# Optimization experiments

Measured on AMD Instinct MI355X. Metric: run time of the kernel, lower is better.

The kernel has to match this reference:

```python
import jax, jax.numpy as jnp
import numpy as np

B, N, HW, PS, FHW = 16, 4096, 224, 8, 56

def _gelu(x):
    return jax.nn.gelu(x, approximate=True)  # tanh approximation, matches nn.GELU(approximate='tanh')

def _conv(x, w, b, stride):
    y = jax.lax.conv_general_dilated(x, w, (stride, stride), [(1, 1), (1, 1)],
                                     dimension_numbers=('NCHW', 'OIHW', 'NCHW'))
    return y + b[None, :, None, None]

def _embed(points):
    # for i in 0..11: append sin(2^i * p) then cos(2^i * p) -> [B,N,48]
    factors = 2.0 ** jnp.arange(12, dtype=points.dtype)
    scaled = points[..., None, :] * factors[:, None]          # [B,N,12,2]
    feats = jnp.concatenate([jnp.sin(scaled), jnp.cos(scaled)], axis=-1)  # [B,N,12,4]
    return feats.reshape(points.shape[0], points.shape[1], 48)

def _extract_patches(fmap, points):
    # fmap [B,C,H,W]; points in [0,1]; bilinear grid_sample, zeros padding, align_corners=True
    Bq, C, H, W = fmap.shape
    centers = points * 2.0 - 1.0
    step = 2.0 / (W - 1)
    half = (PS - 1) / 2.0
    offs = jnp.linspace(-half, half, PS, dtype=fmap.dtype) * step
    offx2d, offy2d = jnp.meshgrid(offs, offs, indexing='ij')   # [ps,ps]
    gx = centers[..., 0][..., None, None] + offx2d             # [B,N,ps,ps]
    gy = centers[..., 1][..., None, None] + offy2d
    # align_corners=True pixel coords
    ix = (gx + 1.0) * 0.5 * (W - 1)
    iy = (gy + 1.0) * 0.5 * (H - 1)
    x0f = jnp.floor(ix); y0f = jnp.floor(iy)
    x0 = x0f.astype(jnp.int32); y0 = y0f.astype(jnp.int32)
    x1 = x0 + 1; y1 = y0 + 1
    wx1 = ix - x0f; wx0 = 1.0 - wx1
    wy1 = iy - y0f; wy0 = 1.0 - wy1
    fflat = fmap.reshape(Bq, C, H * W)

    def corner(xi, yi, w):
        valid = ((xi >= 0) & (xi < W) & (yi >= 0) & (yi < H)).astype(fmap.dtype)
        idx = jnp.clip(yi, 0, H - 1) * W + jnp.clip(xi, 0, W - 1)   # [B,N,ps,ps]
        vals = jax.vmap(lambda f, i: f[:, i])(fflat, idx)           # [B,C,N,ps,ps]
        return vals * (w * valid)[:, None]

    out = (corner(x0, y0, wx0 * wy0) + corner(x1, y0, wx1 * wy0)
           + corner(x0, y1, wx0 * wy1) + corner(x1, y1, wx1 * wy1))  # [B,C,N,ps,ps]
    return out.transpose(0, 2, 1, 3, 4)                              # [B,N,C,ps,ps]

def setup_inputs():
    key = jax.random.key(0)
    ks = jax.random.split(key, 26)
    def w(k, shape):
        fan_in = int(np.prod(shape[1:]))
        return jax.random.normal(k, shape, jnp.float32) * (1.0 / np.sqrt(fan_in))
    inp = {
        'points': jax.random.uniform(ks[0], (B, N, 2), jnp.float32),
        'images': jax.random.normal(ks[1], (B, 3, HW, HW), jnp.float32),
        # plane encoder
        'pw1': w(ks[2], (16, 3, 3, 3)),  'pb1': jnp.zeros((16,), jnp.float32),
        'pw2': w(ks[3], (32, 16, 3, 3)), 'pb2': jnp.zeros((32,), jnp.float32),
        'pw3': w(ks[4], (4, 32, 3, 3)),  'pb3': jnp.zeros((4,), jnp.float32),
        # global encoder
        'gw1': w(ks[5], (4, 3, 3, 3)),   'gb1': jnp.zeros((4,), jnp.float32),
        'gw2': w(ks[6], (8, 4, 3, 3)),   'gb2': jnp.zeros((8,), jnp.float32),
        'gw3': w(ks[7], (16, 8, 3, 3)),  'gb3': jnp.zeros((16,), jnp.float32),
        'gw4': w(ks[8], (32, 16, 3, 3)), 'gb4': jnp.zeros((32,), jnp.float32),
        'gw5': w(ks[9], (64, 32, 3, 3)), 'gb5': jnp.zeros((64,), jnp.float32),
        # point encoder (torch Linear: [out,in])
        'lw1': w(ks[10], (256, 48)),  'lb1': jnp.zeros((256,), jnp.float32),
        'lw2': w(ks[11], (256, 256)), 'lb2': jnp.zeros((256,), jnp.float32),
        # head
        'hw1': w(ks[12], (512, 576)), 'hb1': jnp.zeros((512,), jnp.float32),
        'hw2': w(ks[13], (1, 512)),   'hb2': jnp.zeros((1,), jnp.float32),
    }
    return inp

def reference(points, images, pw1, pb1, pw2, pb2, pw3, pb3,
              gw1, gb1, gw2, gb2, gw3, gb3, gw4, gb4, gw5, gb5,
              lw1, lb1, lw2, lb2, hw1, hb1, hw2, hb2):
    # point branch
    pe = _embed(points)                                         # [B,N,48]
    pf = _gelu(pe @ lw1.T + lb1) @ lw2.T + lb2                  # [B,N,256]
    # plane encoder -> 4x56x56 fmap
    f = _gelu(_conv(images, pw1, pb1, 2))
    f = _gelu(_conv(f, pw2, pb2, 2))
    fmap = _gelu(_conv(f, pw3, pb3, 1))                         # [B,4,56,56]
    # global encoder -> [B,64]
    g = images
    for wg, bg in ((gw1, gb1), (gw2, gb2), (gw3, gb3), (gw4, gb4), (gw5, gb5)):
        g = _gelu(_conv(g, wg, bg, 2))
    gc = g.mean(axis=(2, 3))                                    # AvgPool2d(7)+Flatten -> [B,64]
    gc = jnp.broadcast_to(gc[:, None, :], (points.shape[0], points.shape[1], 64))
    # per-point bilinear patch gather
    patches = _extract_patches(fmap, points).reshape(points.shape[0], points.shape[1], -1)  # [B,N,256]
    fused = jnp.concatenate([pf, patches, gc], axis=-1)         # [B,N,576]
    logit = _gelu(fused @ hw1.T + hb1) @ hw2.T + hb2            # [B,N,1]
    return logit
```

## Files before the change

### kernel.cpp

```cpp
#include <hip/hip_runtime.h>
#include <math.h>

#define BB 16
#define NN 4096
#define M_TOT (BB*NN)
#define TBK 32
#define HBK 64

typedef __attribute__((ext_vector_type(8))) short s8v;
typedef __attribute__((ext_vector_type(4))) float f4v;

__device__ __forceinline__ float gelu_t(float x){
    float u = 1.5957691216057308f * x * (1.0f + 0.044715f*x*x);
    return x / (1.0f + __expf(-u));
}

__device__ __forceinline__ unsigned short f2bf(float f){
    unsigned int u = __float_as_uint(f);
    u += 0x7fffu + ((u >> 16) & 1u);
    return (unsigned short)(u >> 16);
}

#define GLL(src, dst) __builtin_amdgcn_global_load_lds( \
    (const __attribute__((address_space(1))) void*)(src), \
    (__attribute__((address_space(3))) void*)(dst), 16, 0, 0)

template<int CIN, int COUT, int STRIDE, int CHUNK>
__device__ __forceinline__ void conv_dev2(
    const float* __restrict__ in, const float* __restrict__ w,
    const float* __restrict__ bias, float* __restrict__ out,
    int Hin, int Win, int Hout, int Wout, int bx, int by, int b, float* tile)
{
    constexpr int IW = 15*STRIDE + 3;
    constexpr int IH = IW;
    constexpr int PITCH = IW + 1;
    int tid = threadIdx.x;
    int tx = tid & 15, ty = tid >> 4;
    int wo = bx*16 + tx;
    int ho = by*16 + ty;
    int win0 = bx*16*STRIDE - 1;
    int hin0 = by*16*STRIDE - 1;
    bool valid = (wo < Wout) && (ho < Hout);

    float acc[COUT];
    #pragma unroll
    for (int co = 0; co < COUT; ++co) acc[co] = bias[co];

    const float* ib = in + (size_t)(b*CIN)*Hin*Win;
    for (int ci0 = 0; ci0 < CIN; ci0 += CHUNK) {
        __syncthreads();
        for (int idx = tid; idx < CHUNK*IH*IW; idx += 256) {
            int c = idx / (IH*IW), rem = idx - c*(IH*IW);
            int r = rem / IW, cc = rem - r*IW;
            int hi = hin0 + r, wi = win0 + cc;
            float v = 0.f;
            if ((unsigned)hi < (unsigned)Hin && (unsigned)wi < (unsigned)Win)
                v = ib[(size_t)(ci0 + c)*Hin*Win + hi*Win + wi];
            tile[c*IH*PITCH + r*PITCH + cc] = v;
        }
        __syncthreads();
        for (int ci = 0; ci < CHUNK; ++ci) {
            float vv[9];
            const float* tb = tile + ci*IH*PITCH;
            #pragma unroll
            for (int kh = 0; kh < 3; ++kh)
                #pragma unroll
                for (int kw = 0; kw < 3; ++kw)
                    vv[kh*3+kw] = tb[(ty*STRIDE + kh)*PITCH + tx*STRIDE + kw];
            const float* wc = w + (ci0 + ci)*9;
            #pragma unroll
            for (int co = 0; co < COUT; ++co) {
                const float* wp = wc + co*CIN*9;
                #pragma unroll
                for (int k = 0; k < 9; ++k)
                    acc[co] = fmaf(vv[k], wp[k], acc[co]);
            }
        }
    }
    if (valid) {
        size_t obase = ((size_t)b*COUT)*Hout*Wout + (size_t)ho*Wout + wo;
        #pragma unroll
        for (int co = 0; co < COUT; ++co)
            out[obase + (size_t)co*Hout*Wout] = gelu_t(acc[co]);
    }
}

__global__ __launch_bounds__(256) void conv_dual_k(
    const float* __restrict__ in,
    const float* __restrict__ wA, const float* __restrict__ bA,
    const float* __restrict__ wB, const float* __restrict__ bB,
    float* __restrict__ outA, float* __restrict__ outB)
{
    __shared__ float tile[3*33*34];
    const int Hin = 224, Win = 224, Hout = 112, Wout = 112;
    int tid = threadIdx.x;
    int tx = tid & 15, ty = tid >> 4;
    int b = blockIdx.z;
    int wo = blockIdx.x*16 + tx;
    int ho = blockIdx.y*16 + ty;
    int win0 = blockIdx.x*32 - 1;
    int hin0 = blockIdx.y*32 - 1;

    const float* ib = in + (size_t)(b*3)*Hin*Win;
    for (int idx = tid; idx < 3*1089; idx += 256) {
        int c = idx / 1089, rem = idx - c*1089;
        int r = rem / 33, cc = rem - r*33;
        int hi = hin0 + r, wi = win0 + cc;
        float v = 0.f;
        if ((unsigned)hi < (unsigned)Hin && (unsigned)wi < (unsigned)Win)
            v = ib[(size_t)c*Hin*Win + hi*Win + wi];
        tile[c*33*34 + r*34 + cc] = v;
    }
    __syncthreads();

    float accA[16], accB[4];
    #pragma unroll
    for (int co = 0; co < 16; ++co) accA[co] = bA[co];
    #pragma unroll
    for (int co = 0; co < 4; ++co) accB[co] = bB[co];

    #pragma unroll
    for (int ci = 0; ci < 3; ++ci) {
        float vv[9];
        const float* tb = tile + ci*33*34;
        #pragma unroll
        for (int kh = 0; kh < 3; ++kh)
            #pragma unroll
            for (int kw = 0; kw < 3; ++kw)
                vv[kh*3+kw] = tb[(ty*2 + kh)*34 + tx*2 + kw];
        #pragma unroll
        for (int co = 0; co < 16; ++co) {
            const float* wp = wA + co*27 + ci*9;
            #pragma unroll
            for (int k = 0; k < 9; ++k) accA[co] = fmaf(vv[k], wp[k], accA[co]);
        }
        #pragma unroll
        for (int co = 0; co < 4; ++co) {
            const float* wp = wB + co*27 + ci*9;
            #pragma unroll
            for (int k = 0; k < 9; ++k) accB[co] = fmaf(vv[k], wp[k], accB[co]);
        }
    }
    size_t px = (size_t)ho*Wout + wo;
    #pragma unroll
    for (int co = 0; co < 16; ++co)
        outA[((size_t)(b*16 + co))*Hout*Wout + px] = gelu_t(accA[co]);
    #pragma unroll
    for (int co = 0; co < 4; ++co)
        outB[((size_t)(b*4 + co))*Hout*Wout + px] = gelu_t(accB[co]);
}

__global__ __launch_bounds__(256) void conv_pg2_k(
    const float* __restrict__ f1, const float* __restrict__ pw2, const float* __restrict__ pb2, float* __restrict__ f2,
    const float* __restrict__ g1, const float* __restrict__ gw2, const float* __restrict__ gb2, float* __restrict__ g2)
{
    __shared__ float tile[8*33*34];
    int z = blockIdx.z;
    if (z < 32) {
        int b = z >> 1, half = z & 1;
        conv_dev2<16,16,2,8>(f1 + (size_t)b*16*12544, pw2 + half*2304, pb2 + half*16,
                             f2 + ((size_t)(b*32 + half*16))*3136,
                             112,112, 56,56, blockIdx.x, blockIdx.y, 0, tile);
    } else {
        conv_dev2<4,8,2,4>(g1, gw2, gb2, g2, 112,112, 56,56, blockIdx.x, blockIdx.y, z-32, tile);
    }
}

__global__ __launch_bounds__(256) void conv_pg3_k(
    const float* __restrict__ f2, const float* __restrict__ pw3, const float* __restrict__ pb3, float4* __restrict__ fmap4,
    const float* __restrict__ g2, const float* __restrict__ gw3, const float* __restrict__ gb3, float* __restrict__ g3)
{
    __shared__ float tile[8*33*34];
    int z = blockIdx.z;
    if (z < 16) {
        int b = z;
        int idx = blockIdx.x*256 + threadIdx.x;
        if (idx >= 3136) return;
        int ho = idx / 56, wo = idx - ho*56;
        const float* ib = f2 + (size_t)b*32*3136;
        float acc[4];
        #pragma unroll
        for (int co = 0; co < 4; ++co) acc[co] = pb3[co];
        for (int ci = 0; ci < 32; ++ci) {
            const float* ic = ib + (size_t)ci*3136;
            #pragma unroll
            for (int kh = 0; kh < 3; ++kh) {
                int hi = ho - 1 + kh;
                if ((unsigned)hi >= 56u) continue;
                #pragma unroll
                for (int kw = 0; kw < 3; ++kw) {
                    int wi = wo - 1 + kw;
                    if ((unsigned)wi >= 56u) continue;
                    float v = ic[hi*56 + wi];
                    int wofs = ci*9 + kh*3 + kw;
                    #pragma unroll
                    for (int co = 0; co < 4; ++co)
                        acc[co] = fmaf(v, pw3[co*288 + wofs], acc[co]);
                }
            }
        }
        float4 o;
        o.x = gelu_t(acc[0]); o.y = gelu_t(acc[1]);
        o.z = gelu_t(acc[2]); o.w = gelu_t(acc[3]);
        fmap4[(size_t)b*3136 + idx] = o;
    } else {
        if (blockIdx.x >= 4) return;
        int bx = blockIdx.x & 1, by = blockIdx.x >> 1;
        conv_dev2<8,16,2,8>(g2, gw3, gb3, g3, 56,56, 28,28, bx, by, z-16, tile);
    }
}

__global__ __launch_bounds__(256) void g4_k(
    const float* __restrict__ g3, const float* __restrict__ w4,
    const float* __restrict__ b4, float* __restrict__ g4o)
{
    int idx = blockIdx.x*256 + threadIdx.x;
    int co = idx & 31;
    int t = idx >> 5;
    int b = t / 196, px = t - b*196;
    int ho = px / 14, wo = px - ho*14;
    const float* src = g3 + (size_t)b*16*784;
    const float* wp = w4 + co*144;
    float acc = b4[co];
    for (int ci = 0; ci < 16; ++ci) {
        #pragma unroll
        for (int kh = 0; kh < 3; ++kh) {
            int hi = ho*2 - 1 + kh;
            if ((unsigned)hi >= 28u) continue;
            #pragma unroll
            for (int kw = 0; kw < 3; ++kw) {
                int wi = wo*2 - 1 + kw;
                if ((unsigned)wi >= 28u) continue;
                acc = fmaf(src[ci*784 + hi*28 + wi], wp[ci*9 + kh*3 + kw], acc);
            }
        }
    }
    g4o[(size_t)b*6272 + px*32 + co] = gelu_t(acc);
}

__global__ __launch_bounds__(256) void g5_k(
    const float* __restrict__ g4o, const float* __restrict__ w5,
    const float* __restrict__ b5, float* __restrict__ gc)
{
    int idx = blockIdx.x*256 + threadIdx.x;
    int co = idx & 63;
    int t = idx >> 6;
    int b = t / 49, px = t - b*49;
    int ho = px / 7, wo = px - ho*7;
    const float* src = g4o + (size_t)b*6272;
    const float* wp = w5 + co*288;
    float acc = b5[co];
    for (int ci = 0; ci < 32; ++ci) {
        #pragma unroll
        for (int kh = 0; kh < 3; ++kh) {
            int hi = ho*2 - 1 + kh;
            if ((unsigned)hi >= 14u) continue;
            #pragma unroll
            for (int kw = 0; kw < 3; ++kw) {
                int wi = wo*2 - 1 + kw;
                if ((unsigned)wi >= 14u) continue;
                acc = fmaf(src[(hi*14 + wi)*32 + ci], wp[ci*9 + kh*3 + kw], acc);
            }
        }
    }
    atomicAdd(&gc[b*64 + co], gelu_t(acc) * (1.0f/49.0f));
}

__global__ void cvtall_k(const float* __restrict__ lw1, const float* __restrict__ lw2,
                         const float* __restrict__ hw1, unsigned short* __restrict__ blw1,
                         unsigned short* __restrict__ blw2, unsigned short* __restrict__ bhw1,
                         float* __restrict__ out, const float* __restrict__ b2,
                         float* __restrict__ gc){
    int i = blockIdx.x*blockDim.x + threadIdx.x;
    if (i < M_TOT) out[i] = b2[0];
    if (i < 1024) gc[i] = 0.f;
    if (i < 256*64) {
        int r = i >> 6, c = i & 63;
        blw1[i] = (c < 48) ? f2bf(lw1[r*48 + c]) : 0;
        return;
    }
    int j = i - 256*64;
    if (j < 256*256) { blw2[j] = f2bf(lw2[j]); return; }
    j -= 256*256;
    if (j < 512*576) bhw1[j] = f2bf(hw1[j]);
}

__global__ __launch_bounds__(512) void mlp12_k(
    const float* __restrict__ points,
    const unsigned short* __restrict__ W1, const float* __restrict__ b1,
    const unsigned short* __restrict__ W2, const float* __restrict__ b2,
    unsigned short* __restrict__ C,
    const float4* __restrict__ fmap4, const float* __restrict__ gc)
{
    __shared__ unsigned short Hd[128*256];
    int tid = threadIdx.x;
    int wv = tid >> 6, lane = tid & 63;
    int q = lane >> 4, lr = lane & 15;
    int mi = wv >> 2, ni = wv & 3;
    size_t m0 = (size_t)blockIdx.x * 128;

    f4v acc1[4][4];
    #pragma unroll
    for (int i = 0; i < 4; ++i)
        #pragma unroll
        for (int j = 0; j < 4; ++j) acc1[i][j] = (f4v){0.f,0.f,0.f,0.f};

    #pragma unroll
    for (int kb = 0; kb < 2; ++kb) {
        int seg = kb*4 + q;
        s8v a[4], b[4];
        #pragma unroll
        for (int t = 0; t < 4; ++t) {
            size_t m = m0 + mi*64 + t*16 + lr;
            float px = points[m*2], py = points[m*2+1];
            union { s8v v; unsigned short u[8]; } pk;
            #pragma unroll
            for (int j = 0; j < 8; ++j) {
                int k = seg*8 + j;
                unsigned short val = 0;
                if (k < 48) {
                    int i2 = k >> 2, rr = k & 3;
                    float f = (float)(1 << i2);
                    float p = (rr & 1) ? py : px;
                    float s = f * p;
                    val = f2bf((rr < 2) ? __sinf(s) : __cosf(s));
                }
                pk.u[j] = val;
            }
            a[t] = pk.v;
        }
        #pragma unroll
        for (int t = 0; t < 4; ++t) {
            int n = ni*64 + t*16 + lr;
            b[t] = *(const s8v*)(W1 + n*64 + seg*8);
        }
        #pragma unroll
        for (int mt = 0; mt < 4; ++mt)
            #pragma unroll
            for (int nt = 0; nt < 4; ++nt)
                acc1[mt][nt] = __builtin_amdgcn_mfma_f32_16x16x32_bf16(a[mt], b[nt], acc1[mt][nt], 0, 0, 0);
    }
    {
        float b1v[4];
        #pragma unroll
        for (int nt = 0; nt < 4; ++nt) b1v[nt] = b1[ni*64 + nt*16 + lr];
        #pragma unroll
        for (int mt = 0; mt < 4; ++mt)
            #pragma unroll
            for (int r4 = 0; r4 < 4; ++r4) {
                int row = mi*64 + mt*16 + q*4 + r4;
                #pragma unroll
                for (int nt = 0; nt < 4; ++nt) {
                    int col = ni*64 + nt*16 + lr;
                    float v = gelu_t(acc1[mt][nt][r4] + b1v[nt]);
                    int p = (col >> 3) ^ (row & 7);
                    Hd[(row*32 + p)*8 + (col & 7)] = f2bf(v);
                }
            }
    }
    __syncthreads();

    f4v acc2[4][4];
    #pragma unroll
    for (int i = 0; i < 4; ++i)
        #pragma unroll
        for (int j = 0; j < 4; ++j) acc2[i][j] = (f4v){0.f,0.f,0.f,0.f};

    #pragma unroll 2
    for (int kt = 0; kt < 8; ++kt) {
        s8v a[4], b[4];
        #pragma unroll
        for (int t = 0; t < 4; ++t) {
            int n = ni*64 + t*16 + lr;
            b[t] = *(const s8v*)(W2 + (size_t)n*256 + kt*32 + q*8);
        }
        #pragma unroll
        for (int t = 0; t < 4; ++t) {
            int row = mi*64 + t*16 + lr;
            int p = (kt*4 + q) ^ (row & 7);
            a[t] = *(const s8v*)(Hd + (row*32 + p)*8);
        }
        #pragma unroll
        for (int mt = 0; mt < 4; ++mt)
            #pragma unroll
            for (int nt = 0; nt < 4; ++nt)
                acc2[mt][nt] = __builtin_amdgcn_mfma_f32_16x16x32_bf16(a[mt], b[nt], acc2[mt][nt], 0, 0, 0);
    }
    {
        float b2v[4];
        #pragma unroll
        for (int nt = 0; nt < 4; ++nt) b2v[nt] = b2[ni*64 + nt*16 + lr];
        #pragma unroll
        for (int mt = 0; mt < 4; ++mt)
            #pragma unroll
            for (int r4 = 0; r4 < 4; ++r4) {
                size_t m = m0 + mi*64 + mt*16 + q*4 + r4;
                #pragma unroll
                for (int nt = 0; nt < 4; ++nt) {
                    int n = ni*64 + nt*16 + lr;
                    C[m*576 + n] = f2bf(acc2[mt][nt][r4] + b2v[nt]);
                }
            }
    }
    #pragma unroll 2
    for (int it = 0; it < 16; ++it) {
        int task = it*512 + tid;
        int ml = task >> 6, ij = task & 63;
        size_t m = m0 + ml;
        int i = ij >> 3, j = ij & 7;
        int b = (int)(m >> 12);
        float px = points[m*2], py = points[m*2+1];
        float cx = px*2.f - 1.f, cy = py*2.f - 1.f;
        const float step = 2.0f/55.0f;
        float gx = cx + ((float)i - 3.5f)*step;
        float gy = cy + ((float)j - 3.5f)*step;
        float ix = (gx + 1.f)*0.5f*55.f;
        float iy = (gy + 1.f)*0.5f*55.f;
        float x0f = floorf(ix), y0f = floorf(iy);
        int x0 = (int)x0f, y0 = (int)y0f;
        int x1 = x0 + 1,  y1 = y0 + 1;
        float wx1 = ix - x0f, wx0 = 1.f - wx1;
        float wy1 = iy - y0f, wy0 = 1.f - wy1;
        float v00 = ((x0>=0)&&(x0<56)&&(y0>=0)&&(y0<56)) ? 1.f : 0.f;
        float v10 = ((x1>=0)&&(x1<56)&&(y0>=0)&&(y0<56)) ? 1.f : 0.f;
        float v01 = ((x0>=0)&&(x0<56)&&(y1>=0)&&(y1<56)) ? 1.f : 0.f;
        float v11 = ((x1>=0)&&(x1<56)&&(y1>=0)&&(y1<56)) ? 1.f : 0.f;
        float w00 = wx0*wy0*v00, w10 = wx1*wy0*v10, w01 = wx0*wy1*v01, w11 = wx1*wy1*v11;
        int cx0 = min(max(x0,0),55), cx1 = min(max(x1,0),55);
        int cy0 = min(max(y0,0),55), cy1 = min(max(y1,0),55);
        const float4* fb = fmap4 + (size_t)b*3136;
        float4 f00 = fb[cy0*56 + cx0], f10 = fb[cy0*56 + cx1];
        float4 f01 = fb[cy1*56 + cx0], f11 = fb[cy1*56 + cx1];
        float4 v;
        v.x = w00*f00.x + w10*f10.x + w01*f01.x + w11*f11.x;
        v.y = w00*f00.y + w10*f10.y + w01*f01.y + w11*f11.y;
        v.z = w00*f00.z + w10*f10.z + w01*f01.z + w11*f11.z;
        v.w = w00*f00.w + w10*f10.w + w01*f01.w + w11*f11.w;
        C[m*576 + 256 +   0 + ij] = f2bf(v.x);
        C[m*576 + 256 +  64 + ij] = f2bf(v.y);
        C[m*576 + 256 + 128 + ij] = f2bf(v.z);
        C[m*576 + 256 + 192 + ij] = f2bf(v.w);
        C[m*576 + 512 + ij] = f2bf(gc[b*64 + ij]);
    }
}

__global__ __launch_bounds__(256, 3) void gemm_hd_k(
    const unsigned short* __restrict__ A,
    const unsigned short* __restrict__ W,
    const float* __restrict__ bias, const float* __restrict__ w2,
    float* __restrict__ out)
{
    __shared__ unsigned short As[64*HBK];
    __shared__ unsigned short Bs[256*HBK];
    __shared__ float red[4*64];
    int tid = threadIdx.x;
    int wv = tid >> 6, lane = tid & 63;
    int q = lane >> 4, lr = lane & 15;
    int nq = wv * 64;
    size_t m0 = (size_t)blockIdx.x * 64;
    int nbase = blockIdx.y * 256;

    const unsigned short* srcA[2]; unsigned short* dstA[2];
    #pragma unroll
    for (int r = 0; r < 2; ++r) {
        int f = r*256 + tid;
        int row = f >> 3, sl = (f & 7) ^ (row & 7);
        srcA[r] = A + (m0 + row)*576 + sl*8;
        dstA[r] = As + f*8;
    }
    const unsigned short* srcB[8]; unsigned short* dstB[8];
    #pragma unroll
    for (int r = 0; r < 8; ++r) {
        int f = r*256 + tid;
        int row = f >> 3, sl = (f & 7) ^ (row & 7);
        srcB[r] = W + (size_t)(nbase + row)*576 + sl*8;
        dstB[r] = Bs + f*8;
    }

    f4v acc[4][4];
    #pragma unroll
    for (int i = 0; i < 4; ++i)
        #pragma unroll
        for (int j = 0; j < 4; ++j) acc[i][j] = (f4v){0.f,0.f,0.f,0.f};

    for (int k0 = 0; k0 < 576; k0 += HBK) {
        #pragma unroll
        for (int r = 0; r < 2; ++r) { GLL(srcA[r], dstA[r]); srcA[r] += HBK; }
        #pragma unroll
        for (int r = 0; r < 8; ++r) { GLL(srcB[r], dstB[r]); srcB[r] += HBK; }
        __syncthreads();
        #pragma unroll
        for (int kk = 0; kk < 2; ++kk) {
            s8v a[4], b[4];
            #pragma unroll
            for (int t = 0; t < 4; ++t) {
                int row = t*16 + lr;
                int ph = (kk*4 + q) ^ (row & 7);
                a[t] = *(const s8v*)(As + (row*8 + ph)*8);
            }
            #pragma unroll
            for (int t = 0; t < 4; ++t) {
                int row = nq + t*16 + lr;
                int ph = (kk*4 + q) ^ (row & 7);
                b[t] = *(const s8v*)(Bs + (row*8 + ph)*8);
            }
            #pragma unroll
            for (int mt = 0; mt < 4; ++mt)
                #pragma unroll
                for (int nt = 0; nt < 4; ++nt)
                    acc[mt][nt] = __builtin_amdgcn_mfma_f32_16x16x32_bf16(a[mt], b[nt], acc[mt][nt], 0, 0, 0);
        }
        __syncthreads();
    }
    float bv[4], w2v[4];
    #pragma unroll
    for (int nt = 0; nt < 4; ++nt) {
        int n = nbase + nq + nt*16 + lr;
        bv[nt] = bias[n];
        w2v[nt] = w2[n];
    }
    #pragma unroll
    for (int mt = 0; mt < 4; ++mt)
        #pragma unroll
        for (int r4 = 0; r4 < 4; ++r4) {
            int ml = mt*16 + q*4 + r4;
            float s = 0.f;
            #pragma unroll
            for (int nt = 0; nt < 4; ++nt)
                s += gelu_t(acc[mt][nt][r4] + bv[nt]) * w2v[nt];
            #pragma unroll
            for (int off = 8; off > 0; off >>= 1) s += __shfl_down(s, off, 16);
            if (lr == 0) red[wv*64 + ml] = s;
        }
    __syncthreads();
    if (tid < 64) {
        float t = red[tid] + red[64 + tid] + red[128 + tid] + red[192 + tid];
        atomicAdd(&out[m0 + tid], t);
    }
}

extern "C" void kernel_launch(void* const* d_in, const int* in_sizes, int n_in,
                              void* d_out, int out_size, void* d_ws, size_t ws_size,
                              hipStream_t stream) {
    const float* points = (const float*)d_in[0];
    const float* images = (const float*)d_in[1];
    const float* pw1 = (const float*)d_in[2];  const float* pb1 = (const float*)d_in[3];
    const float* pw2 = (const float*)d_in[4];  const float* pb2 = (const float*)d_in[5];
    const float* pw3 = (const float*)d_in[6];  const float* pb3 = (const float*)d_in[7];
    const float* gw1 = (const float*)d_in[8];  const float* gb1 = (const float*)d_in[9];
    const float* gw2 = (const float*)d_in[10]; const float* gb2 = (const float*)d_in[11];
    const float* gw3 = (const float*)d_in[12]; const float* gb3 = (const float*)d_in[13];
    const float* gw4 = (const float*)d_in[14]; const float* gb4 = (const float*)d_in[15];
    const float* gw5 = (const float*)d_in[16]; const float* gb5 = (const float*)d_in[17];
    const float* lw1 = (const float*)d_in[18]; const float* lb1 = (const float*)d_in[19];
    const float* lw2 = (const float*)d_in[20]; const float* lb2 = (const float*)d_in[21];
    const float* hw1 = (const float*)d_in[22]; const float* hb1 = (const float*)d_in[23];
    const float* hw2 = (const float*)d_in[24]; const float* hb2 = (const float*)d_in[25];
    float* out = (float*)d_out;

    char* base = (char*)d_ws;
    unsigned short* fused_b = (unsigned short*)base;
    unsigned short* hid_b   = fused_b + (size_t)M_TOT*576;
    float4* fmap4 = (float4*)(hid_b + (size_t)M_TOT*256);
    float* gc   = (float*)(fmap4 + (size_t)16*3136);
    unsigned short* blw1 = (unsigned short*)(gc + 1024);
    unsigned short* blw2 = blw1 + 256*64;
    unsigned short* bhw1 = blw2 + 256*256;
    float* ct = (float*)base;
    float* f1 = ct;
    float* f2 = f1 + (size_t)16*16*112*112;
    float* g1 = f2 + (size_t)16*32*56*56;
    float* g2 = g1 + (size_t)16*4*112*112;
    float* g3 = g2 + (size_t)16*8*56*56;
    float* g4 = g3 + (size_t)16*16*28*28;

    cvtall_k<<<1472, 256, 0, stream>>>(lw1, lw2, hw1, blw1, blw2, bhw1, out, hb2, gc);
    conv_dual_k<<<dim3(7,7,16), 256, 0, stream>>>(images, pw1, pb1, gw1, gb1, f1, g1);
    conv_pg2_k<<<dim3(4,4,48), 256, 0, stream>>>(f1, pw2, pb2, f2, g1, gw2, gb2, g2);
    conv_pg3_k<<<dim3(13,1,32), 256, 0, stream>>>(f2, pw3, pb3, fmap4, g2, gw3, gb3, g3);
    g4_k<<<392, 256, 0, stream>>>(g3, gw4, gb4, g4);
    g5_k<<<196, 256, 0, stream>>>(g4, gw5, gb5, gc);
    mlp12_k<<<M_TOT/128, 512, 0, stream>>>(points, blw1, lb1, blw2, lb2, fused_b, fmap4, gc);
    gemm_hd_k<<<dim3(M_TOT/64, 2), 256, 0, stream>>>(fused_b, bhw1, hb1, hw2, out);
}
```

Measured before the change: 429.3 us.

## Fold global-context columns into per-image bias and co-schedule MLP with convs

The 64 global-context columns of the head GEMM are constant per image, so their product with hw1 plus hb1 is precomputed once per image into a bias table (hgc_k). This shrinks the fused activation row from 576 to 512 and cuts the head GEMM's K loop and the write and read traffic of the fused buffer. The point MLP is merged into the first conv kernel as extra blocks and the patch gather into the g4 conv kernel, so small, under-occupied conv launches overlap with independent work. It adds one small kernel launch, and the MLP blocks now use 64-row tiles.

```diff
diff --git a/kernel.cpp b/kernel.cpp
--- a/kernel.cpp
+++ b/kernel.cpp
@@ -85,69 +85,186 @@
     }
 }
 
-__global__ __launch_bounds__(256) void conv_dual_k(
-    const float* __restrict__ in,
-    const float* __restrict__ wA, const float* __restrict__ bA,
-    const float* __restrict__ wB, const float* __restrict__ bB,
-    float* __restrict__ outA, float* __restrict__ outB)
-{
-    __shared__ float tile[3*33*34];
-    const int Hin = 224, Win = 224, Hout = 112, Wout = 112;
+__global__ __launch_bounds__(256) void k1_k(
+    const float* __restrict__ images,
+    const float* __restrict__ pw1, const float* __restrict__ pb1,
+    const float* __restrict__ gw1, const float* __restrict__ gb1,
+    float* __restrict__ f1, float* __restrict__ g1,
+    const float* __restrict__ points,
+    const unsigned short* __restrict__ W1, const float* __restrict__ b1,
+    const unsigned short* __restrict__ W2, const float* __restrict__ b2,
+    unsigned short* __restrict__ C)
+{
+    __shared__ char smem[32768];
+    int bid = blockIdx.x;
     int tid = threadIdx.x;
-    int tx = tid & 15, ty = tid >> 4;
-    int b = blockIdx.z;
-    int wo = blockIdx.x*16 + tx;
-    int ho = blockIdx.y*16 + ty;
-    int win0 = blockIdx.x*32 - 1;
-    int hin0 = blockIdx.y*32 - 1;
-
-    const float* ib = in + (size_t)(b*3)*Hin*Win;
-    for (int idx = tid; idx < 3*1089; idx += 256) {
-        int c = idx / 1089, rem = idx - c*1089;
-        int r = rem / 33, cc = rem - r*33;
-        int hi = hin0 + r, wi = win0 + cc;
-        float v = 0.f;
-        if ((unsigned)hi < (unsigned)Hin && (unsigned)wi < (unsigned)Win)
-            v = ib[(size_t)c*Hin*Win + hi*Win + wi];
-        tile[c*33*34 + r*34 + cc] = v;
-    }
-    __syncthreads();
-
-    float accA[16], accB[4];
-    #pragma unroll
-    for (int co = 0; co < 16; ++co) accA[co] = bA[co];
-    #pragma unroll
-    for (int co = 0; co < 4; ++co) accB[co] = bB[co];
-
-    #pragma unroll
-    for (int ci = 0; ci < 3; ++ci) {
-        float vv[9];
-        const float* tb = tile + ci*33*34;
-        #pragma unroll
-        for (int kh = 0; kh < 3; ++kh)
-            #pragma unroll
-            for (int kw = 0; kw < 3; ++kw)
-                vv[kh*3+kw] = tb[(ty*2 + kh)*34 + tx*2 + kw];
-        #pragma unroll
-        for (int co = 0; co < 16; ++co) {
-            const float* wp = wA + co*27 + ci*9;
-            #pragma unroll
-            for (int k = 0; k < 9; ++k) accA[co] = fmaf(vv[k], wp[k], accA[co]);
-        }
-        #pragma unroll
-        for (int co = 0; co < 4; ++co) {
-            const float* wp = wB + co*27 + ci*9;
-            #pragma unroll
-            for (int k = 0; k < 9; ++k) accB[co] = fmaf(vv[k], wp[k], accB[co]);
-        }
-    }
-    size_t px = (size_t)ho*Wout + wo;
-    #pragma unroll
-    for (int co = 0; co < 16; ++co)
-        outA[((size_t)(b*16 + co))*Hout*Wout + px] = gelu_t(accA[co]);
-    #pragma unroll
-    for (int co = 0; co < 4; ++co)
-        outB[((size_t)(b*4 + co))*Hout*Wout + px] = gelu_t(accB[co]);
+    if (bid < 784) {
+        float* tile = (float*)smem;
+        const int Hin = 224, Win = 224, Hout = 112, Wout = 112;
+        int b = bid / 49, rem = bid - b*49;
+        int by = rem / 7, bx = rem - by*7;
+        int tx = tid & 15, ty = tid >> 4;
+        int wo = bx*16 + tx;
+        int ho = by*16 + ty;
+        int win0 = bx*32 - 1;
+        int hin0 = by*32 - 1;
+
+        const float* ib = images + (size_t)(b*3)*Hin*Win;
+        for (int idx = tid; idx < 3*1089; idx += 256) {
+            int c = idx / 1089, r2 = idx - c*1089;
+            int r = r2 / 33, cc = r2 - r*33;
+            int hi = hin0 + r, wi = win0 + cc;
+            float v = 0.f;
+            if ((unsigned)hi < (unsigned)Hin && (unsigned)wi < (unsigned)Win)
+                v = ib[(size_t)c*Hin*Win + hi*Win + wi];
+            tile[c*33*34 + r*34 + cc] = v;
+        }
+        __syncthreads();
+
+        float accA[16], accB[4];
+        #pragma unroll
+        for (int co = 0; co < 16; ++co) accA[co] = pb1[co];
+        #pragma unroll
+        for (int co = 0; co < 4; ++co) accB[co] = gb1[co];
+
+        #pragma unroll
+        for (int ci = 0; ci < 3; ++ci) {
+            float vv[9];
+            const float* tb = tile + ci*33*34;
+            #pragma unroll
+            for (int kh = 0; kh < 3; ++kh)
+                #pragma unroll
+                for (int kw = 0; kw < 3; ++kw)
+                    vv[kh*3+kw] = tb[(ty*2 + kh)*34 + tx*2 + kw];
+            #pragma unroll
+            for (int co = 0; co < 16; ++co) {
+                const float* wp = pw1 + co*27 + ci*9;
+                #pragma unroll
+                for (int k = 0; k < 9; ++k) accA[co] = fmaf(vv[k], wp[k], accA[co]);
+            }
+            #pragma unroll
+            for (int co = 0; co < 4; ++co) {
+                const float* wp = gw1 + co*27 + ci*9;
+                #pragma unroll
+                for (int k = 0; k < 9; ++k) accB[co] = fmaf(vv[k], wp[k], accB[co]);
+            }
+        }
+        size_t px = (size_t)ho*Wout + wo;
+        #pragma unroll
+        for (int co = 0; co < 16; ++co)
+            f1[((size_t)(b*16 + co))*Hout*Wout + px] = gelu_t(accA[co]);
+        #pragma unroll
+        for (int co = 0; co < 4; ++co)
+            g1[((size_t)(b*4 + co))*Hout*Wout + px] = gelu_t(accB[co]);
+    } else {
+        unsigned short* Hd = (unsigned short*)smem;
+        int wv = tid >> 6, lane = tid & 63;
+        int q = lane >> 4, lr = lane & 15;
+        int nq = wv * 64;
+        size_t m0 = (size_t)(bid - 784) * 64;
+
+        f4v acc1[4][4];
+        #pragma unroll
+        for (int i = 0; i < 4; ++i)
+            #pragma unroll
+            for (int j = 0; j < 4; ++j) acc1[i][j] = (f4v){0.f,0.f,0.f,0.f};
+
+        #pragma unroll
+        for (int kb = 0; kb < 2; ++kb) {
+            int seg = kb*4 + q;
+            s8v a[4], b[4];
+            #pragma unroll
+            for (int t = 0; t < 4; ++t) {
+                size_t m = m0 + t*16 + lr;
+                float px = points[m*2], py = points[m*2+1];
+                union { s8v v; unsigned short u[8]; } pk;
+                #pragma unroll
+                for (int j = 0; j < 8; ++j) {
+                    int k = seg*8 + j;
+                    unsigned short val = 0;
+                    if (k < 48) {
+                        int i2 = k >> 2, rr = k & 3;
+                        float f = (float)(1 << i2);
+                        float p = (rr & 1) ? py : px;
+                        float s = f * p;
+                        val = f2bf((rr < 2) ? __sinf(s) : __cosf(s));
+                    }
+                    pk.u[j] = val;
+                }
+                a[t] = pk.v;
+            }
+            #pragma unroll
+            for (int t = 0; t < 4; ++t) {
+                int n = nq + t*16 + lr;
+                b[t] = *(const s8v*)(W1 + n*64 + seg*8);
+            }
+            #pragma unroll
+            for (int mt = 0; mt < 4; ++mt)
+                #pragma unroll
+                for (int nt = 0; nt < 4; ++nt)
+                    acc1[mt][nt] = __builtin_amdgcn_mfma_f32_16x16x32_bf16(a[mt], b[nt], acc1[mt][nt], 0, 0, 0);
+        }
+        {
+            float b1v[4];
+            #pragma unroll
+            for (int nt = 0; nt < 4; ++nt) b1v[nt] = b1[nq + nt*16 + lr];
+            #pragma unroll
+            for (int mt = 0; mt < 4; ++mt)
+                #pragma unroll
+                for (int r4 = 0; r4 < 4; ++r4) {
+                    int row = mt*16 + q*4 + r4;
+                    #pragma unroll
+                    for (int nt = 0; nt < 4; ++nt) {
+                        int col = nq + nt*16 + lr;
+                        float v = gelu_t(acc1[mt][nt][r4] + b1v[nt]);
+                        int p = (col >> 3) ^ (row & 7);
+                        Hd[(row*32 + p)*8 + (col & 7)] = f2bf(v);
+                    }
+                }
+        }
+        __syncthreads();
+
+        f4v acc2[4][4];
+        #pragma unroll
+        for (int i = 0; i < 4; ++i)
+            #pragma unroll
+            for (int j = 0; j < 4; ++j) acc2[i][j] = (f4v){0.f,0.f,0.f,0.f};
+
+        #pragma unroll 2
+        for (int kt = 0; kt < 8; ++kt) {
+            s8v a[4], b[4];
+            #pragma unroll
+            for (int t = 0; t < 4; ++t) {
+                int n = nq + t*16 + lr;
+                b[t] = *(const s8v*)(W2 + (size_t)n*256 + kt*32 + q*8);
+            }
+            #pragma unroll
+            for (int t = 0; t < 4; ++t) {
+                int row = t*16 + lr;
+                int p = (kt*4 + q) ^ (row & 7);
+                a[t] = *(const s8v*)(Hd + (row*32 + p)*8);
+            }
+            #pragma unroll
+            for (int mt = 0; mt < 4; ++mt)
+                #pragma unroll
+                for (int nt = 0; nt < 4; ++nt)
+                    acc2[mt][nt] = __builtin_amdgcn_mfma_f32_16x16x32_bf16(a[mt], b[nt], acc2[mt][nt], 0, 0, 0);
+        }
+        float b2v[4];
+        #pragma unroll
+        for (int nt = 0; nt < 4; ++nt) b2v[nt] = b2[nq + nt*16 + lr];
+        #pragma unroll
+        for (int mt = 0; mt < 4; ++mt)
+            #pragma unroll
+            for (int r4 = 0; r4 < 4; ++r4) {
+                size_t m = m0 + mt*16 + q*4 + r4;
+                #pragma unroll
+                for (int nt = 0; nt < 4; ++nt) {
+                    int n = nq + nt*16 + lr;
+                    C[m*512 + n] = f2bf(acc2[mt][nt][r4] + b2v[nt]);
+                }
+            }
+    }
 }
 
 __global__ __launch_bounds__(256) void conv_pg2_k(
@@ -210,203 +327,41 @@
     }
 }
 
-__global__ __launch_bounds__(256) void g4_k(
+__global__ __launch_bounds__(256) void k4_k(
     const float* __restrict__ g3, const float* __restrict__ w4,
-    const float* __restrict__ b4, float* __restrict__ g4o)
-{
-    int idx = blockIdx.x*256 + threadIdx.x;
-    int co = idx & 31;
-    int t = idx >> 5;
-    int b = t / 196, px = t - b*196;
-    int ho = px / 14, wo = px - ho*14;
-    const float* src = g3 + (size_t)b*16*784;
-    const float* wp = w4 + co*144;
-    float acc = b4[co];
-    for (int ci = 0; ci < 16; ++ci) {
-        #pragma unroll
-        for (int kh = 0; kh < 3; ++kh) {
-            int hi = ho*2 - 1 + kh;
-            if ((unsigned)hi >= 28u) continue;
-            #pragma unroll
-            for (int kw = 0; kw < 3; ++kw) {
-                int wi = wo*2 - 1 + kw;
-                if ((unsigned)wi >= 28u) continue;
-                acc = fmaf(src[ci*784 + hi*28 + wi], wp[ci*9 + kh*3 + kw], acc);
-            }
-        }
-    }
-    g4o[(size_t)b*6272 + px*32 + co] = gelu_t(acc);
-}
-
-__global__ __launch_bounds__(256) void g5_k(
-    const float* __restrict__ g4o, const float* __restrict__ w5,
-    const float* __restrict__ b5, float* __restrict__ gc)
-{
-    int idx = blockIdx.x*256 + threadIdx.x;
-    int co = idx & 63;
-    int t = idx >> 6;
-    int b = t / 49, px = t - b*49;
-    int ho = px / 7, wo = px - ho*7;
-    const float* src = g4o + (size_t)b*6272;
-    const float* wp = w5 + co*288;
-    float acc = b5[co];
-    for (int ci = 0; ci < 32; ++ci) {
-        #pragma unroll
-        for (int kh = 0; kh < 3; ++kh) {
-            int hi = ho*2 - 1 + kh;
-            if ((unsigned)hi >= 14u) continue;
-            #pragma unroll
-            for (int kw = 0; kw < 3; ++kw) {
-                int wi = wo*2 - 1 + kw;
-                if ((unsigned)wi >= 14u) continue;
-                acc = fmaf(src[(hi*14 + wi)*32 + ci], wp[ci*9 + kh*3 + kw], acc);
-            }
-        }
-    }
-    atomicAdd(&gc[b*64 + co], gelu_t(acc) * (1.0f/49.0f));
-}
-
-__global__ void cvtall_k(const float* __restrict__ lw1, const float* __restrict__ lw2,
-                         const float* __restrict__ hw1, unsigned short* __restrict__ blw1,
-                         unsigned short* __restrict__ blw2, unsigned short* __restrict__ bhw1,
-                         float* __restrict__ out, const float* __restrict__ b2,
-                         float* __restrict__ gc){
-    int i = blockIdx.x*blockDim.x + threadIdx.x;
-    if (i < M_TOT) out[i] = b2[0];
-    if (i < 1024) gc[i] = 0.f;
-    if (i < 256*64) {
-        int r = i >> 6, c = i & 63;
-        blw1[i] = (c < 48) ? f2bf(lw1[r*48 + c]) : 0;
-        return;
-    }
-    int j = i - 256*64;
-    if (j < 256*256) { blw2[j] = f2bf(lw2[j]); return; }
-    j -= 256*256;
-    if (j < 512*576) bhw1[j] = f2bf(hw1[j]);
-}
-
-__global__ __launch_bounds__(512) void mlp12_k(
-    const float* __restrict__ points,
-    const unsigned short* __restrict__ W1, const float* __restrict__ b1,
-    const unsigned short* __restrict__ W2, const float* __restrict__ b2,
-    unsigned short* __restrict__ C,
-    const float4* __restrict__ fmap4, const float* __restrict__ gc)
-{
-    __shared__ unsigned short Hd[128*256];
+    const float* __restrict__ b4, float* __restrict__ g4o,
+    const float4* __restrict__ fmap4, const float* __restrict__ points,
+    unsigned short* __restrict__ C)
+{
+    int bid = blockIdx.x;
     int tid = threadIdx.x;
-    int wv = tid >> 6, lane = tid & 63;
-    int q = lane >> 4, lr = lane & 15;
-    int mi = wv >> 2, ni = wv & 3;
-    size_t m0 = (size_t)blockIdx.x * 128;
-
-    f4v acc1[4][4];
-    #pragma unroll
-    for (int i = 0; i < 4; ++i)
-        #pragma unroll
-        for (int j = 0; j < 4; ++j) acc1[i][j] = (f4v){0.f,0.f,0.f,0.f};
-
-    #pragma unroll
-    for (int kb = 0; kb < 2; ++kb) {
-        int seg = kb*4 + q;
-        s8v a[4], b[4];
-        #pragma unroll
-        for (int t = 0; t < 4; ++t) {
-            size_t m = m0 + mi*64 + t*16 + lr;
-            float px = points[m*2], py = points[m*2+1];
-            union { s8v v; unsigned short u[8]; } pk;
-            #pragma unroll
-            for (int j = 0; j < 8; ++j) {
-                int k = seg*8 + j;
-                unsigned short val = 0;
-                if (k < 48) {
-                    int i2 = k >> 2, rr = k & 3;
-                    float f = (float)(1 << i2);
-                    float p = (rr & 1) ? py : px;
-                    float s = f * p;
-                    val = f2bf((rr < 2) ? __sinf(s) : __cosf(s));
+    if (bid < 392) {
+        int idx = bid*256 + tid;
+        int co = idx & 31;
+        int t = idx >> 5;
+        int b = t / 196, px = t - b*196;
+        int ho = px / 14, wo = px - ho*14;
+        const float* src = g3 + (size_t)b*16*784;
+        const float* wp = w4 + co*144;
+        float acc = b4[co];
+        for (int ci = 0; ci < 16; ++ci) {
+            #pragma unroll
+            for (int kh = 0; kh < 3; ++kh) {
+                int hi = ho*2 - 1 + kh;
+                if ((unsigned)hi >= 28u) continue;
+                #pragma unroll
+                for (int kw = 0; kw < 3; ++kw) {
+                    int wi = wo*2 - 1 + kw;
+                    if ((unsigned)wi >= 28u) continue;
+                    acc = fmaf(src[ci*784 + hi*28 + wi], wp[ci*9 + kh*3 + kw], acc);
                 }
-                pk.u[j] = val;
-            }
-            a[t] = pk.v;
-        }
-        #pragma unroll
-        for (int t = 0; t < 4; ++t) {
-            int n = ni*64 + t*16 + lr;
-            b[t] = *(const s8v*)(W1 + n*64 + seg*8);
-        }
-        #pragma unroll
-        for (int mt = 0; mt < 4; ++mt)
-            #pragma unroll
-            for (int nt = 0; nt < 4; ++nt)
-                acc1[mt][nt] = __builtin_amdgcn_mfma_f32_16x16x32_bf16(a[mt], b[nt], acc1[mt][nt], 0, 0, 0);
-    }
-    {
-        float b1v[4];
-        #pragma unroll
-        for (int nt = 0; nt < 4; ++nt) b1v[nt] = b1[ni*64 + nt*16 + lr];
-        #pragma unroll
-        for (int mt = 0; mt < 4; ++mt)
-            #pragma unroll
-            for (int r4 = 0; r4 < 4; ++r4) {
-                int row = mi*64 + mt*16 + q*4 + r4;
-                #pragma unroll
-                for (int nt = 0; nt < 4; ++nt) {
-                    int col = ni*64 + nt*16 + lr;
-                    float v = gelu_t(acc1[mt][nt][r4] + b1v[nt]);
-                    int p = (col >> 3) ^ (row & 7);
-                    Hd[(row*32 + p)*8 + (col & 7)] = f2bf(v);
-                }
-            }
-    }
-    __syncthreads();
-
-    f4v acc2[4][4];
-    #pragma unroll
-    for (int i = 0; i < 4; ++i)
-        #pragma unroll
-        for (int j = 0; j < 4; ++j) acc2[i][j] = (f4v){0.f,0.f,0.f,0.f};
-
-    #pragma unroll 2
-    for (int kt = 0; kt < 8; ++kt) {
-        s8v a[4], b[4];
-        #pragma unroll
-        for (int t = 0; t < 4; ++t) {
-            int n = ni*64 + t*16 + lr;
-            b[t] = *(const s8v*)(W2 + (size_t)n*256 + kt*32 + q*8);
-        }
-        #pragma unroll
-        for (int t = 0; t < 4; ++t) {
-            int row = mi*64 + t*16 + lr;
-            int p = (kt*4 + q) ^ (row & 7);
-            a[t] = *(const s8v*)(Hd + (row*32 + p)*8);
-        }
-        #pragma unroll
-        for (int mt = 0; mt < 4; ++mt)
-            #pragma unroll
-            for (int nt = 0; nt < 4; ++nt)
-                acc2[mt][nt] = __builtin_amdgcn_mfma_f32_16x16x32_bf16(a[mt], b[nt], acc2[mt][nt], 0, 0, 0);
-    }
-    {
-        float b2v[4];
-        #pragma unroll
-        for (int nt = 0; nt < 4; ++nt) b2v[nt] = b2[ni*64 + nt*16 + lr];
-        #pragma unroll
-        for (int mt = 0; mt < 4; ++mt)
-            #pragma unroll
-            for (int r4 = 0; r4 < 4; ++r4) {
-                size_t m = m0 + mi*64 + mt*16 + q*4 + r4;
-                #pragma unroll
-                for (int nt = 0; nt < 4; ++nt) {
-                    int n = ni*64 + nt*16 + lr;
-                    C[m*576 + n] = f2bf(acc2[mt][nt][r4] + b2v[nt]);
-                }
-            }
-    }
-    #pragma unroll 2
-    for (int it = 0; it < 16; ++it) {
-        int task = it*512 + tid;
+            }
+        }
+        g4o[(size_t)b*6272 + px*32 + co] = gelu_t(acc);
+    } else {
+        int task = (bid - 392)*256 + tid;
         int ml = task >> 6, ij = task & 63;
-        size_t m = m0 + ml;
+        size_t m = (size_t)ml;
         int i = ij >> 3, j = ij & 7;
         int b = (int)(m >> 12);
         float px = points[m*2], py = points[m*2+1];
@@ -436,18 +391,78 @@
         v.y = w00*f00.y + w10*f10.y + w01*f01.y + w11*f11.y;
         v.z = w00*f00.z + w10*f10.z + w01*f01.z + w11*f11.z;
         v.w = w00*f00.w + w10*f10.w + w01*f01.w + w11*f11.w;
-        C[m*576 + 256 +   0 + ij] = f2bf(v.x);
-        C[m*576 + 256 +  64 + ij] = f2bf(v.y);
-        C[m*576 + 256 + 128 + ij] = f2bf(v.z);
-        C[m*576 + 256 + 192 + ij] = f2bf(v.w);
-        C[m*576 + 512 + ij] = f2bf(gc[b*64 + ij]);
-    }
+        C[m*512 + 256 +   0 + ij] = f2bf(v.x);
+        C[m*512 + 256 +  64 + ij] = f2bf(v.y);
+        C[m*512 + 256 + 128 + ij] = f2bf(v.z);
+        C[m*512 + 256 + 192 + ij] = f2bf(v.w);
+    }
+}
+
+__global__ __launch_bounds__(256) void g5_k(
+    const float* __restrict__ g4o, const float* __restrict__ w5,
+    const float* __restrict__ b5, float* __restrict__ gc)
+{
+    int idx = blockIdx.x*256 + threadIdx.x;
+    int co = idx & 63;
+    int t = idx >> 6;
+    int b = t / 49, px = t - b*49;
+    int ho = px / 7, wo = px - ho*7;
+    const float* src = g4o + (size_t)b*6272;
+    const float* wp = w5 + co*288;
+    float acc = b5[co];
+    for (int ci = 0; ci < 32; ++ci) {
+        #pragma unroll
+        for (int kh = 0; kh < 3; ++kh) {
+            int hi = ho*2 - 1 + kh;
+            if ((unsigned)hi >= 14u) continue;
+            #pragma unroll
+            for (int kw = 0; kw < 3; ++kw) {
+                int wi = wo*2 - 1 + kw;
+                if ((unsigned)wi >= 14u) continue;
+                acc = fmaf(src[(hi*14 + wi)*32 + ci], wp[ci*9 + kh*3 + kw], acc);
+            }
+        }
+    }
+    atomicAdd(&gc[b*64 + co], gelu_t(acc) * (1.0f/49.0f));
+}
+
+__global__ __launch_bounds__(256) void hgc_k(
+    const float* __restrict__ gc, const float* __restrict__ hw1,
+    const float* __restrict__ hb1, float* __restrict__ hgc)
+{
+    int idx = blockIdx.x*256 + threadIdx.x;
+    int b = idx >> 9, n = idx & 511;
+    const float* g = gc + b*64;
+    const float* w = hw1 + (size_t)n*576 + 512;
+    float s = hb1[n];
+    #pragma unroll
+    for (int c = 0; c < 64; ++c) s = fmaf(g[c], w[c], s);
+    hgc[idx] = s;
+}
+
+__global__ void cvtall_k(const float* __restrict__ lw1, const float* __restrict__ lw2,
+                         const float* __restrict__ hw1, unsigned short* __restrict__ blw1,
+                         unsigned short* __restrict__ blw2, unsigned short* __restrict__ bhw1,
+                         float* __restrict__ out, const float* __restrict__ b2,
+                         float* __restrict__ gc){
+    int i = blockIdx.x*blockDim.x + threadIdx.x;
+    if (i < M_TOT) out[i] = b2[0];
+    if (i < 1024) gc[i] = 0.f;
+    if (i < 256*64) {
+        int r = i >> 6, c = i & 63;
+        blw1[i] = (c < 48) ? f2bf(lw1[r*48 + c]) : 0;
+        return;
+    }
+    int j = i - 256*64;
+    if (j < 256*256) { blw2[j] = f2bf(lw2[j]); return; }
+    j -= 256*256;
+    if (j < 512*576) bhw1[j] = f2bf(hw1[j]);
 }
 
 __global__ __launch_bounds__(256, 3) void gemm_hd_k(
     const unsigned short* __restrict__ A,
     const unsigned short* __restrict__ W,
-    const float* __restrict__ bias, const float* __restrict__ w2,
+    const float* __restrict__ hgc, const float* __restrict__ w2,
     float* __restrict__ out)
 {
     __shared__ unsigned short As[64*HBK];
@@ -459,13 +474,14 @@
     int nq = wv * 64;
     size_t m0 = (size_t)blockIdx.x * 64;
     int nbase = blockIdx.y * 256;
+    int bimg = (int)(m0 >> 12);
 
     const unsigned short* srcA[2]; unsigned short* dstA[2];
     #pragma unroll
     for (int r = 0; r < 2; ++r) {
         int f = r*256 + tid;
         int row = f >> 3, sl = (f & 7) ^ (row & 7);
-        srcA[r] = A + (m0 + row)*576 + sl*8;
+        srcA[r] = A + (m0 + row)*512 + sl*8;
         dstA[r] = As + f*8;
     }
     const unsigned short* srcB[8]; unsigned short* dstB[8];
@@ -483,7 +499,7 @@
         #pragma unroll
         for (int j = 0; j < 4; ++j) acc[i][j] = (f4v){0.f,0.f,0.f,0.f};
 
-    for (int k0 = 0; k0 < 576; k0 += HBK) {
+    for (int k0 = 0; k0 < 512; k0 += HBK) {
         #pragma unroll
         for (int r = 0; r < 2; ++r) { GLL(srcA[r], dstA[r]); srcA[r] += HBK; }
         #pragma unroll
@@ -516,7 +532,7 @@
     #pragma unroll
     for (int nt = 0; nt < 4; ++nt) {
         int n = nbase + nq + nt*16 + lr;
-        bv[nt] = bias[n];
+        bv[nt] = hgc[bimg*512 + n];
         w2v[nt] = w2[n];
     }
     #pragma unroll
@@ -560,26 +576,27 @@
 
     char* base = (char*)d_ws;
     unsigned short* fused_b = (unsigned short*)base;
-    unsigned short* hid_b   = fused_b + (size_t)M_TOT*576;
-    float4* fmap4 = (float4*)(hid_b + (size_t)M_TOT*256);
-    float* gc   = (float*)(fmap4 + (size_t)16*3136);
-    unsigned short* blw1 = (unsigned short*)(gc + 1024);
-    unsigned short* blw2 = blw1 + 256*64;
-    unsigned short* bhw1 = blw2 + 256*256;
-    float* ct = (float*)base;
-    float* f1 = ct;
+    float* conv = (float*)(fused_b + (size_t)M_TOT*512);
+    float* f1 = conv;
     float* f2 = f1 + (size_t)16*16*112*112;
     float* g1 = f2 + (size_t)16*32*56*56;
     float* g2 = g1 + (size_t)16*4*112*112;
     float* g3 = g2 + (size_t)16*8*56*56;
     float* g4 = g3 + (size_t)16*16*28*28;
+    float4* fmap4 = (float4*)(g4 + (size_t)16*32*14*14);
+    float* gc   = (float*)(fmap4 + (size_t)16*3136);
+    float* hgc  = gc + 1024;
+    unsigned short* blw1 = (unsigned short*)(hgc + 16*512);
+    unsigned short* blw2 = blw1 + 256*64;
+    unsigned short* bhw1 = blw2 + 256*256;
 
     cvtall_k<<<1472, 256, 0, stream>>>(lw1, lw2, hw1, blw1, blw2, bhw1, out, hb2, gc);
-    conv_dual_k<<<dim3(7,7,16), 256, 0, stream>>>(images, pw1, pb1, gw1, gb1, f1, g1);
+    k1_k<<<784 + 1024, 256, 0, stream>>>(images, pw1, pb1, gw1, gb1, f1, g1,
+                                         points, blw1, lb1, blw2, lb2, fused_b);
     conv_pg2_k<<<dim3(4,4,48), 256, 0, stream>>>(f1, pw2, pb2, f2, g1, gw2, gb2, g2);
     conv_pg3_k<<<dim3(13,1,32), 256, 0, stream>>>(f2, pw3, pb3, fmap4, g2, gw3, gb3, g3);
-    g4_k<<<392, 256, 0, stream>>>(g3, gw4, gb4, g4);
+    k4_k<<<392 + 16384, 256, 0, stream>>>(g3, gw4, gb4, g4, fmap4, points, fused_b);
     g5_k<<<196, 256, 0, stream>>>(g4, gw5, gb5, gc);
-    mlp12_k<<<M_TOT/128, 512, 0, stream>>>(points, blw1, lb1, blw2, lb2, fused_b, fmap4, gc);
-    gemm_hd_k<<<dim3(M_TOT/64, 2), 256, 0, stream>>>(fused_b, bhw1, hb1, hw2, out);
-}
+    hgc_k<<<32, 256, 0, stream>>>(gc, hw1, hb1, hgc);
+    gemm_hd_k<<<dim3(M_TOT/64, 2), 256, 0, stream>>>(fused_b, bhw1, hgc, hw2, out);
+}
```

Measured after the change: 449.5 us. +4.7%, slower.
